# Performance work log

Hardware: AMD Instinct MI355X
Metric: run time of the kernel (lower is better)

The kernel has to match this reference:

```python
import jax, jax.numpy as jnp
import numpy as np

D_MODEL = 2048
N_HEADS = 16
HEAD_DIM = 128
ROPE_THETA = 10000.0


def _rope_cache(seq_len, dim, theta):
    inv_freq = 1.0 / (theta ** (jnp.arange(0, dim, 2, dtype=jnp.float32) / dim))
    t = jnp.arange(seq_len, dtype=jnp.float32)
    freqs = jnp.outer(t, inv_freq)          # [T, dim/2]
    emb = jnp.concatenate([freqs, freqs], axis=-1)  # [T, dim]
    return jnp.cos(emb), jnp.sin(emb)


def _rotate_half(x):
    d = x.shape[-1] // 2
    return jnp.concatenate([-x[..., d:], x[..., :d]], axis=-1)


def setup_inputs() -> dict:
    key = jax.random.key(0)
    k1, k2, k3 = jax.random.split(key, 3)
    B, T, D = 2, 2048, D_MODEL
    x = jax.random.normal(k1, (B, T, D), dtype=jnp.float32)
    w_qkv = jax.random.normal(k2, (D, 3 * D), dtype=jnp.float32) * (D ** -0.5)
    w_out = jax.random.normal(k3, (D, D), dtype=jnp.float32) * (D ** -0.5)
    return {"x": x, "w_qkv": w_qkv, "w_out": w_out}


def reference(x, w_qkv, w_out):
    B, T, D = x.shape
    H, Hd = N_HEADS, HEAD_DIM
    qkv = x @ w_qkv                                  # [B, T, 3D]
    q, k, v = jnp.split(qkv, 3, axis=-1)
    # [B, H, T, Hd]
    q = q.reshape(B, T, H, Hd).transpose(0, 2, 1, 3)
    k = k.reshape(B, T, H, Hd).transpose(0, 2, 1, 3)
    v = v.reshape(B, T, H, Hd).transpose(0, 2, 1, 3)
    cos, sin = _rope_cache(T, Hd, ROPE_THETA)        # [T, Hd]
    cos = cos[None, None]                            # [1,1,T,Hd]
    sin = sin[None, None]
    q = q * cos + _rotate_half(q) * sin
    k = k * cos + _rotate_half(k) * sin
    scale = Hd ** -0.5
    logits = jnp.einsum('bhqd,bhkd->bhqk', q, k) * scale
    causal = jnp.tril(jnp.ones((T, T), dtype=bool))
    logits = jnp.where(causal[None, None], logits, jnp.finfo(logits.dtype).min)
    attn = jax.nn.softmax(logits, axis=-1)
    out = jnp.einsum('bhqk,bhkd->bhqd', attn, v)     # [B,H,T,Hd]
    out = out.transpose(0, 2, 1, 3).reshape(B, T, D)
    return out @ w_out
```

## Files before the change

### kernel.cpp

```cpp
#include <hip/hip_runtime.h>

typedef unsigned short u16;
typedef unsigned int u32;
typedef __bf16 bf16x8 __attribute__((ext_vector_type(8)));
typedef float f32x4 __attribute__((ext_vector_type(4)));
typedef u16 u16x4 __attribute__((ext_vector_type(4)));
typedef u16 u16x8 __attribute__((ext_vector_type(8)));

#define T_SEQ 2048
#define DMODEL 2048
#define NQKV 6144
#define HD 128
#define NH 16
#define MROWS 4096

__device__ __forceinline__ u16 f2b(float f) {
  union { float f; u32 u; } a; a.f = f;
  u32 r = a.u + 0x7fffu + ((a.u >> 16) & 1u);
  return (u16)(r >> 16);
}
__device__ __forceinline__ float b2f(u16 h) {
  union { u32 u; float f; } a; a.u = ((u32)h) << 16;
  return a.f;
}
__device__ __forceinline__ void g2l16(const u16* g, u16* l) {
  __builtin_amdgcn_global_load_lds((const __attribute__((address_space(1))) u32*)g,
                                   (__attribute__((address_space(3))) u32*)l, 16, 0, 0);
}

__global__ void k_f32_to_bf16(const float* __restrict__ in, u16* __restrict__ out, int n) {
  int i = (blockIdx.x * 256 + threadIdx.x) * 8;
  if (i >= n) return;
  float4 a = *(const float4*)(in + i);
  float4 b = *(const float4*)(in + i + 4);
  u16x8 v;
  v[0] = f2b(a.x); v[1] = f2b(a.y); v[2] = f2b(a.z); v[3] = f2b(a.w);
  v[4] = f2b(b.x); v[5] = f2b(b.y); v[6] = f2b(b.z); v[7] = f2b(b.w);
  *(u16x8*)(out + i) = v;
}

__global__ void k_transpose_bf16(const float* __restrict__ in, u16* __restrict__ out,
                                 int R, int C) {
  __shared__ u16 tile[32][33];
  const int c0 = blockIdx.x * 32, r0 = blockIdx.y * 32;
  const int tx = threadIdx.x & 31, ty = threadIdx.x >> 5;
#pragma unroll
  for (int i = 0; i < 32; i += 8)
    tile[ty + i][tx] = f2b(in[(size_t)(r0 + ty + i) * C + c0 + tx]);
  __syncthreads();
#pragma unroll
  for (int i = 0; i < 32; i += 8)
    out[(size_t)(c0 + ty + i) * R + r0 + tx] = tile[tx][ty + i];
}

__global__ void k_rope_cache(float* __restrict__ cosb, float* __restrict__ sinb) {
  int idx = blockIdx.x * 256 + threadIdx.x;
  int t = idx >> 6, d = idx & 63;
  float inv = powf(10000.0f, -(float)d * (1.0f / 64.0f));
  float fr = (float)t * inv;
  cosb[idx] = cosf(fr);
  sinb[idx] = sinf(fr);
}

__global__ __launch_bounds__(256) void k_gemm_qkv(const u16* __restrict__ A,
                                                  const u16* __restrict__ B,
                                                  const float* __restrict__ cosb,
                                                  const float* __restrict__ sinb,
                                                  u16* __restrict__ qr,
                                                  u16* __restrict__ kr,
                                                  u16* __restrict__ vtb) {
  __shared__ __align__(16) u16 lA[128 * 64];
  __shared__ __align__(16) u16 lB[128 * 64];
  const int K = DMODEL;
  const int tid = threadIdx.x;
  const int wid = tid >> 6, lane = tid & 63;
  const int g = lane >> 4, q = lane & 15;
  const int wr = wid >> 1, wc = wid & 1;
  const int bn = blockIdx.x, bm = blockIdx.y;
  const int l8 = lane >> 3, l7 = lane & 7;
  const f32x4 fzero = {0.f, 0.f, 0.f, 0.f};
  f32x4 acc[4][4];
#pragma unroll
  for (int m = 0; m < 4; ++m)
#pragma unroll
    for (int n = 0; n < 4; ++n) acc[m][n] = fzero;

  const u16* Ab = A + (size_t)bm * 128 * K;
  const u16* Bb = B + (size_t)bn * 128 * K;

  for (int k0 = 0; k0 < K; k0 += 64) {
    __syncthreads();
#pragma unroll
    for (int i = 0; i < 4; ++i) {
      int chunk = wid * 4 + i;
      int row = chunk * 8 + l8;
      int scol = (l7 * 8) ^ ((row & 7) << 3);
      g2l16(Ab + (size_t)row * K + k0 + scol, lA + chunk * 512);
      g2l16(Bb + (size_t)row * K + k0 + scol, lB + chunk * 512);
    }
    __syncthreads();
#pragma unroll
    for (int kk = 0; kk < 2; ++kk) {
      bf16x8 af[4], bfr[4];
#pragma unroll
      for (int m = 0; m < 4; ++m) {
        int row = wr * 64 + m * 16 + q;
        int col = (kk * 32 + g * 8) ^ ((row & 7) << 3);
        af[m] = *(const bf16x8*)(lA + row * 64 + col);
      }
#pragma unroll
      for (int n = 0; n < 4; ++n) {
        int row = wc * 32 + (n & 1) * 16 + (n >> 1) * 64 + q;
        int col = (kk * 32 + g * 8) ^ ((row & 7) << 3);
        bfr[n] = *(const bf16x8*)(lB + row * 64 + col);
      }
#pragma unroll
      for (int m = 0; m < 4; ++m)
#pragma unroll
        for (int n = 0; n < 4; ++n)
          acc[m][n] = __builtin_amdgcn_mfma_f32_16x16x32_bf16(af[m], bfr[n], acc[m][n], 0, 0, 0);
    }
  }

  const int h = bn & 15;
  const int which = bn >> 4;
  const int b = bm >> 4;
  const int bh = b * 16 + h;
  const int tb0 = (bm & 15) * 128 + wr * 64;
  const float qscale = 0.08838834764831845f;

  if (which == 2) {
    u16* vdst = vtb + (size_t)bh * HD * T_SEQ;
#pragma unroll
    for (int m = 0; m < 4; ++m)
#pragma unroll
      for (int n = 0; n < 4; ++n) {
        int c = wc * 32 + (n & 1) * 16 + (n >> 1) * 64 + q;
        int t0 = tb0 + m * 16 + g * 4;
        u16x4 pk;
#pragma unroll
        for (int r = 0; r < 4; ++r) pk[r] = f2b(acc[m][n][r]);
        *(u16x4*)(vdst + (size_t)c * T_SEQ + t0) = pk;
      }
  } else {
    u16* dst = (which ? kr : qr) + (size_t)bh * T_SEQ * HD;
    const float sc = which ? 1.0f : qscale;
#pragma unroll
    for (int m = 0; m < 4; ++m)
#pragma unroll
      for (int n = 0; n < 2; ++n) {
        int dm = wc * 32 + n * 16 + q;
#pragma unroll
        for (int r = 0; r < 4; ++r) {
          int t = tb0 + m * 16 + g * 4 + r;
          float cv = cosb[t * 64 + dm];
          float sv = sinb[t * 64 + dm];
          float x0 = acc[m][n][r];
          float x1 = acc[m][n + 2][r];
          dst[(size_t)t * HD + dm] = f2b((x0 * cv - x1 * sv) * sc);
          dst[(size_t)t * HD + 64 + dm] = f2b((x1 * cv + x0 * sv) * sc);
        }
      }
  }
}

template <int EPI>
__global__ __launch_bounds__(256) void k_gemm_nt(const u16* __restrict__ A,
                                                 const u16* __restrict__ B,
                                                 void* __restrict__ Cv,
                                                 int M, int N, int K) {
  __shared__ __align__(16) u16 lA[128 * 64];
  __shared__ __align__(16) u16 lB[128 * 64];
  const int tid = threadIdx.x;
  const int wid = tid >> 6, lane = tid & 63;
  const int g = lane >> 4, q = lane & 15;
  const int wr = wid >> 1, wc = wid & 1;
  const int bn = blockIdx.x, bm = blockIdx.y;
  const int l8 = lane >> 3, l7 = lane & 7;
  const f32x4 fzero = {0.f, 0.f, 0.f, 0.f};
  f32x4 acc[4][4];
#pragma unroll
  for (int m = 0; m < 4; ++m)
#pragma unroll
    for (int n = 0; n < 4; ++n) acc[m][n] = fzero;

  const u16* Ab = A + (size_t)bm * 128 * K;
  const u16* Bb = B + (size_t)bn * 128 * K;

  for (int k0 = 0; k0 < K; k0 += 64) {
    __syncthreads();
#pragma unroll
    for (int i = 0; i < 4; ++i) {
      int chunk = wid * 4 + i;
      int row = chunk * 8 + l8;
      int scol = (l7 * 8) ^ ((row & 7) << 3);
      g2l16(Ab + (size_t)row * K + k0 + scol, lA + chunk * 512);
      g2l16(Bb + (size_t)row * K + k0 + scol, lB + chunk * 512);
    }
    __syncthreads();
#pragma unroll
    for (int kk = 0; kk < 2; ++kk) {
      bf16x8 af[4], bfr[4];
#pragma unroll
      for (int m = 0; m < 4; ++m) {
        int row = wr * 64 + m * 16 + q;
        int col = (kk * 32 + g * 8) ^ ((row & 7) << 3);
        af[m] = *(const bf16x8*)(lA + row * 64 + col);
      }
#pragma unroll
      for (int n = 0; n < 4; ++n) {
        int row = wc * 64 + n * 16 + q;
        int col = (kk * 32 + g * 8) ^ ((row & 7) << 3);
        bfr[n] = *(const bf16x8*)(lB + row * 64 + col);
      }
#pragma unroll
      for (int m = 0; m < 4; ++m)
#pragma unroll
        for (int n = 0; n < 4; ++n)
          acc[m][n] = __builtin_amdgcn_mfma_f32_16x16x32_bf16(af[m], bfr[n], acc[m][n], 0, 0, 0);
    }
  }
  const int rbase = bm * 128 + wr * 64;
  const int cbase = bn * 128 + wc * 64;
#pragma unroll
  for (int m = 0; m < 4; ++m)
#pragma unroll
    for (int n = 0; n < 4; ++n) {
      int col = cbase + n * 16 + q;
#pragma unroll
      for (int r = 0; r < 4; ++r) {
        int row = rbase + m * 16 + g * 4 + r;
        if (EPI == 0)
          ((u16*)Cv)[(size_t)row * N + col] = f2b(acc[m][n][r]);
        else
          ((float*)Cv)[(size_t)row * N + col] = acc[m][n][r];
      }
    }
}

__global__ __launch_bounds__(256) void k_attn(const u16* __restrict__ qr,
                                              const u16* __restrict__ kr,
                                              const u16* __restrict__ vtb,
                                              u16* __restrict__ ao) {
  __shared__ __align__(16) u16 lK[64 * 128];
  __shared__ __align__(16) u16 lV[128 * 64];
  __shared__ __align__(16) u16 lP[4][16 * 72];
  const int bh = blockIdx.x, b = bh >> 4, h = bh & 15;
  const int qt = (T_SEQ / 64 - 1) - blockIdx.y;
  const int tid = threadIdx.x;
  const int wid = tid >> 6, lane = tid & 63;
  const int g = lane >> 4, q = lane & 15;
  const int qw0 = qt * 64 + wid * 16;
  const u16* qb = qr + (size_t)bh * T_SEQ * HD;
  const u16* kbp = kr + (size_t)bh * T_SEQ * HD;
  const u16* vb = vtb + (size_t)bh * HD * T_SEQ;
  const f32x4 fzero = {0.f, 0.f, 0.f, 0.f};

  bf16x8 qf[4];
#pragma unroll
  for (int ks = 0; ks < 4; ++ks)
    qf[ks] = *(const bf16x8*)(qb + (size_t)(qw0 + q) * HD + ks * 32 + g * 8);

  f32x4 o_acc[8];
#pragma unroll
  for (int n = 0; n < 8; ++n) o_acc[n] = fzero;
  float m_run = -1e30f, l_run = 0.f;

  const int ntiles = qt + 1;
  for (int kt = 0; kt < ntiles; ++kt) {
    const int kb = kt * 64;
    __syncthreads();
#pragma unroll
    for (int i = 0; i < 4; ++i) {
      int chunk = wid * 4 + i;
      int row = chunk * 4 + g;
      int scol = (q * 8) ^ ((row & 7) << 3);
      g2l16(kbp + (size_t)(kb + row) * HD + scol, lK + chunk * 512);
    }
#pragma unroll
    for (int i = 0; i < 4; ++i) {
      int chunk = wid * 4 + i;
      int row = chunk * 8 + (lane >> 3);
      int scol = ((lane & 7) * 8) ^ ((row & 7) << 3);
      g2l16(vb + (size_t)row * T_SEQ + kb + scol, lV + chunk * 512);
    }
    __syncthreads();
    {
      f32x4 st[4];
#pragma unroll
      for (int m = 0; m < 4; ++m) st[m] = fzero;
#pragma unroll
      for (int ks = 0; ks < 4; ++ks) {
#pragma unroll
        for (int m = 0; m < 4; ++m) {
          int row = m * 16 + q;
          int col = (ks * 32 + g * 8) ^ ((row & 7) << 3);
          bf16x8 kf = *(const bf16x8*)(lK + row * 128 + col);
          st[m] = __builtin_amdgcn_mfma_f32_16x16x32_bf16(kf, qf[ks], st[m], 0, 0, 0);
        }
      }
      const int qrow = qw0 + q;
      float p[4][4];
      float pmax = -1e30f;
#pragma unroll
      for (int m = 0; m < 4; ++m)
#pragma unroll
        for (int r = 0; r < 4; ++r) {
          int kcol = kb + m * 16 + g * 4 + r;
          float s = (kcol <= qrow) ? st[m][r] : -1e30f;
          p[m][r] = s;
          pmax = fmaxf(pmax, s);
        }
      pmax = fmaxf(pmax, __shfl_xor(pmax, 16));
      pmax = fmaxf(pmax, __shfl_xor(pmax, 32));
      float m_new = fmaxf(m_run, pmax);
      float corr = __expf(m_run - m_new);
      float ls = 0.f;
#pragma unroll
      for (int m = 0; m < 4; ++m)
#pragma unroll
        for (int r = 0; r < 4; ++r) {
          float e = __expf(p[m][r] - m_new);
          p[m][r] = e;
          ls += e;
        }
      ls += __shfl_xor(ls, 16);
      ls += __shfl_xor(ls, 32);
      l_run = l_run * corr + ls;
      m_run = m_new;
#pragma unroll
      for (int m = 0; m < 4; ++m) {
#pragma unroll
        for (int rp = 0; rp < 2; ++rp) {
          u32 pk = (u32)f2b(p[m][rp * 2]) | ((u32)f2b(p[m][rp * 2 + 1]) << 16);
          *(u32*)(&lP[wid][q * 72 + m * 16 + g * 4 + rp * 2]) = pk;
        }
      }
      asm volatile("s_waitcnt lgkmcnt(0)" ::: "memory");
      __builtin_amdgcn_sched_barrier(0);
      float corr4[4];
#pragma unroll
      for (int r = 0; r < 4; ++r) corr4[r] = __shfl(corr, g * 4 + r);
#pragma unroll
      for (int n = 0; n < 8; ++n) {
#pragma unroll
        for (int r = 0; r < 4; ++r) o_acc[n][r] *= corr4[r];
      }
#pragma unroll
      for (int ks = 0; ks < 2; ++ks) {
        bf16x8 pf = *(const bf16x8*)(&lP[wid][q * 72 + ks * 32 + g * 8]);
#pragma unroll
        for (int n = 0; n < 8; ++n) {
          int row = n * 16 + q;
          int col = (ks * 32 + g * 8) ^ ((row & 7) << 3);
          bf16x8 vf = *(const bf16x8*)(lV + row * 64 + col);
          o_acc[n] = __builtin_amdgcn_mfma_f32_16x16x32_bf16(pf, vf, o_acc[n], 0, 0, 0);
        }
      }
    }
  }
  float linv[4];
#pragma unroll
  for (int r = 0; r < 4; ++r) {
    float lv = __shfl(l_run, g * 4 + r);
    linv[r] = 1.0f / lv;
  }
#pragma unroll
  for (int n = 0; n < 8; ++n)
#pragma unroll
    for (int r = 0; r < 4; ++r) {
      int trow = qw0 + g * 4 + r;
      ao[(size_t)(b * T_SEQ + trow) * DMODEL + h * HD + n * 16 + q] = f2b(o_acc[n][r] * linv[r]);
    }
}

extern "C" void kernel_launch(void* const* d_in, const int* in_sizes, int n_in,
                              void* d_out, int out_size, void* d_ws, size_t ws_size,
                              hipStream_t stream) {
  const float* x = (const float*)d_in[0];
  const float* w_qkv = (const float*)d_in[1];
  const float* w_out = (const float*)d_in[2];
  char* ws = (char*)d_ws;
  size_t off = 0;
  u16* xb = (u16*)(ws + off);    off += (size_t)MROWS * DMODEL * 2;
  u16* wqkvT = (u16*)(ws + off); off += (size_t)NQKV * DMODEL * 2;
  u16* woutT = (u16*)(ws + off); off += (size_t)DMODEL * DMODEL * 2;
  u16* qr = (u16*)(ws + off);    off += (size_t)32 * T_SEQ * HD * 2;
  u16* kr = (u16*)(ws + off);    off += (size_t)32 * T_SEQ * HD * 2;
  u16* vtb = (u16*)(ws + off);   off += (size_t)32 * T_SEQ * HD * 2;
  float* cosb = (float*)(ws + off); off += (size_t)T_SEQ * 64 * 4;
  float* sinb = (float*)(ws + off); off += (size_t)T_SEQ * 64 * 4;
  u16* ao = xb;

  k_f32_to_bf16<<<dim3(MROWS * DMODEL / (256 * 8)), 256, 0, stream>>>(x, xb, MROWS * DMODEL);
  k_transpose_bf16<<<dim3(NQKV / 32, DMODEL / 32), 256, 0, stream>>>(w_qkv, wqkvT, DMODEL, NQKV);
  k_transpose_bf16<<<dim3(DMODEL / 32, DMODEL / 32), 256, 0, stream>>>(w_out, woutT, DMODEL, DMODEL);
  k_rope_cache<<<dim3(T_SEQ * 64 / 256), 256, 0, stream>>>(cosb, sinb);
  k_gemm_qkv<<<dim3(NQKV / 128, MROWS / 128), 256, 0, stream>>>(xb, wqkvT, cosb, sinb, qr, kr, vtb);
  k_attn<<<dim3(32, T_SEQ / 64), 256, 0, stream>>>(qr, kr, vtb, ao);
  k_gemm_nt<1><<<dim3(DMODEL / 128, MROWS / 128), 256, 0, stream>>>(ao, woutT, d_out, MROWS, DMODEL, DMODEL);
}
```

Baseline: 264.9 us.

## Widen attention query tiles, swizzle blocks across XCDs, interleave RoPE cos/sin

```diff
diff --git a/kernel.cpp b/kernel.cpp
--- a/kernel.cpp
+++ b/kernel.cpp
@@ -53,19 +53,18 @@
     out[(size_t)(c0 + ty + i) * R + r0 + tx] = tile[tx][ty + i];
 }
 
-__global__ void k_rope_cache(float* __restrict__ cosb, float* __restrict__ sinb) {
+__global__ void k_rope_cache(float* __restrict__ csb) {
   int idx = blockIdx.x * 256 + threadIdx.x;
   int t = idx >> 6, d = idx & 63;
   float inv = powf(10000.0f, -(float)d * (1.0f / 64.0f));
   float fr = (float)t * inv;
-  cosb[idx] = cosf(fr);
-  sinb[idx] = sinf(fr);
+  float2 cs = make_float2(cosf(fr), sinf(fr));
+  *(float2*)(csb + (size_t)idx * 2) = cs;
 }
 
 __global__ __launch_bounds__(256) void k_gemm_qkv(const u16* __restrict__ A,
                                                   const u16* __restrict__ B,
-                                                  const float* __restrict__ cosb,
-                                                  const float* __restrict__ sinb,
+                                                  const float* __restrict__ csb,
                                                   u16* __restrict__ qr,
                                                   u16* __restrict__ kr,
                                                   u16* __restrict__ vtb) {
@@ -76,7 +75,9 @@
   const int wid = tid >> 6, lane = tid & 63;
   const int g = lane >> 4, q = lane & 15;
   const int wr = wid >> 1, wc = wid & 1;
-  const int bn = blockIdx.x, bm = blockIdx.y;
+  const int lin = blockIdx.y * 48 + blockIdx.x;
+  const int id2 = (lin & 7) * 192 + (lin >> 3);
+  const int bn = id2 % 48, bm = id2 / 48;
   const int l8 = lane >> 3, l7 = lane & 7;
   const f32x4 fzero = {0.f, 0.f, 0.f, 0.f};
   f32x4 acc[4][4];
@@ -153,12 +154,12 @@
 #pragma unroll
         for (int r = 0; r < 4; ++r) {
           int t = tb0 + m * 16 + g * 4 + r;
-          float cv = cosb[t * 64 + dm];
-          float sv = sinb[t * 64 + dm];
+          float2 cs = *(const float2*)(csb + ((size_t)t * 64 + dm) * 2);
           float x0 = acc[m][n][r];
           float x1 = acc[m][n + 2][r];
-          dst[(size_t)t * HD + dm] = f2b((x0 * cv - x1 * sv) * sc);
-          dst[(size_t)t * HD + 64 + dm] = f2b((x1 * cv + x0 * sv) * sc);
+          u32 pk = (u32)f2b((x0 * cs.x - x1 * cs.y) * sc) |
+                   ((u32)f2b((x1 * cs.x + x0 * cs.y) * sc) << 16);
+          *(u32*)(dst + (size_t)t * HD + dm * 2) = pk;
         }
       }
   }
@@ -175,7 +176,11 @@
   const int wid = tid >> 6, lane = tid & 63;
   const int g = lane >> 4, q = lane & 15;
   const int wr = wid >> 1, wc = wid & 1;
-  const int bn = blockIdx.x, bm = blockIdx.y;
+  const int gx = gridDim.x;
+  const int lin = blockIdx.y * gx + blockIdx.x;
+  const int cpx = (gx * gridDim.y) >> 3;
+  const int id2 = (lin & 7) * cpx + (lin >> 3);
+  const int bn = id2 % gx, bm = id2 / gx;
   const int l8 = lane >> 3, l7 = lane & 7;
   const f32x4 fzero = {0.f, 0.f, 0.f, 0.f};
   f32x4 acc[4][4];
@@ -238,19 +243,22 @@
     }
 }
 
-__global__ __launch_bounds__(256) void k_attn(const u16* __restrict__ qr,
+__global__ __launch_bounds__(512) void k_attn(const u16* __restrict__ qr,
                                               const u16* __restrict__ kr,
                                               const u16* __restrict__ vtb,
                                               u16* __restrict__ ao) {
   __shared__ __align__(16) u16 lK[64 * 128];
   __shared__ __align__(16) u16 lV[128 * 64];
-  __shared__ __align__(16) u16 lP[4][16 * 72];
-  const int bh = blockIdx.x, b = bh >> 4, h = bh & 15;
-  const int qt = (T_SEQ / 64 - 1) - blockIdx.y;
+  __shared__ __align__(16) u16 lP[8][16 * 72];
+  const int lin = blockIdx.y * 32 + blockIdx.x;
+  const int id2 = (lin & 7) * 64 + (lin >> 3);
+  const int bh = id2 >> 4, b = bh >> 4, h = bh & 15;
+  const int qt = 15 - (id2 & 15);
   const int tid = threadIdx.x;
   const int wid = tid >> 6, lane = tid & 63;
   const int g = lane >> 4, q = lane & 15;
-  const int qw0 = qt * 64 + wid * 16;
+  const int l8 = lane >> 3, l7 = lane & 7;
+  const int qw0 = qt * 128 + wid * 16;
   const u16* qb = qr + (size_t)bh * T_SEQ * HD;
   const u16* kbp = kr + (size_t)bh * T_SEQ * HD;
   const u16* vb = vtb + (size_t)bh * HD * T_SEQ;
@@ -266,22 +274,22 @@
   for (int n = 0; n < 8; ++n) o_acc[n] = fzero;
   float m_run = -1e30f, l_run = 0.f;
 
-  const int ntiles = qt + 1;
+  const int ntiles = 2 * qt + 2;
   for (int kt = 0; kt < ntiles; ++kt) {
     const int kb = kt * 64;
     __syncthreads();
 #pragma unroll
-    for (int i = 0; i < 4; ++i) {
-      int chunk = wid * 4 + i;
+    for (int i = 0; i < 2; ++i) {
+      int chunk = wid * 2 + i;
       int row = chunk * 4 + g;
       int scol = (q * 8) ^ ((row & 7) << 3);
       g2l16(kbp + (size_t)(kb + row) * HD + scol, lK + chunk * 512);
     }
 #pragma unroll
-    for (int i = 0; i < 4; ++i) {
-      int chunk = wid * 4 + i;
-      int row = chunk * 8 + (lane >> 3);
-      int scol = ((lane & 7) * 8) ^ ((row & 7) << 3);
+    for (int i = 0; i < 2; ++i) {
+      int chunk = wid * 2 + i;
+      int row = chunk * 8 + l8;
+      int scol = (l7 * 8) ^ ((row & 7) << 3);
       g2l16(vb + (size_t)row * T_SEQ + kb + scol, lV + chunk * 512);
     }
     __syncthreads();
@@ -388,15 +396,14 @@
   u16* qr = (u16*)(ws + off);    off += (size_t)32 * T_SEQ * HD * 2;
   u16* kr = (u16*)(ws + off);    off += (size_t)32 * T_SEQ * HD * 2;
   u16* vtb = (u16*)(ws + off);   off += (size_t)32 * T_SEQ * HD * 2;
-  float* cosb = (float*)(ws + off); off += (size_t)T_SEQ * 64 * 4;
-  float* sinb = (float*)(ws + off); off += (size_t)T_SEQ * 64 * 4;
+  float* csb = (float*)(ws + off); off += (size_t)T_SEQ * 64 * 2 * 4;
   u16* ao = xb;
 
   k_f32_to_bf16<<<dim3(MROWS * DMODEL / (256 * 8)), 256, 0, stream>>>(x, xb, MROWS * DMODEL);
   k_transpose_bf16<<<dim3(NQKV / 32, DMODEL / 32), 256, 0, stream>>>(w_qkv, wqkvT, DMODEL, NQKV);
   k_transpose_bf16<<<dim3(DMODEL / 32, DMODEL / 32), 256, 0, stream>>>(w_out, woutT, DMODEL, DMODEL);
-  k_rope_cache<<<dim3(T_SEQ * 64 / 256), 256, 0, stream>>>(cosb, sinb);
-  k_gemm_qkv<<<dim3(NQKV / 128, MROWS / 128), 256, 0, stream>>>(xb, wqkvT, cosb, sinb, qr, kr, vtb);
-  k_attn<<<dim3(32, T_SEQ / 64), 256, 0, stream>>>(qr, kr, vtb, ao);
+  k_rope_cache<<<dim3(T_SEQ * 64 / 256), 256, 0, stream>>>(csb);
+  k_gemm_qkv<<<dim3(48, 32), 256, 0, stream>>>(xb, wqkvT, csb, qr, kr, vtb);
+  k_attn<<<dim3(32, 16), 512, 0, stream>>>(qr, kr, vtb, ao);
   k_gemm_nt<1><<<dim3(DMODEL / 128, MROWS / 128), 256, 0, stream>>>(ao, woutT, d_out, MROWS, DMODEL, DMODEL);
 }
```

After: 300.3 us. +13.4%, slower.
